# Kernel tuning notes

Hardware: AMD Instinct MI355X
Metric: run time of the kernel (lower is better)

The kernel has to match this reference:

```python
import jax, jax.numpy as jnp
import numpy as np

D_MODEL = 256
N_HEADS = 8
WS = 4          # window size
SHIFTED = True
HEAD_DIM = D_MODEL // N_HEADS


def _shift_masks(ws):
    # Masks for the last row / last column of windows after the cyclic shift
    # (standard from-scratch Swin shifted-window mask construction).
    T = ws * ws
    s = ws * (ws // 2)
    row = np.zeros((T, T), np.float32)
    row[-s:, :-s] = -np.inf
    row[:-s, -s:] = -np.inf
    # einops '(r w1) (c w2) -> (w1 r) (w2 c)' with w1=w2=ws
    col = row.reshape(ws, ws, ws, ws).transpose(1, 0, 3, 2).reshape(T, T)
    return jnp.asarray(row), jnp.asarray(col)


def setup_inputs() -> dict:
    key = jax.random.key(0)
    kx, kw, kb = jax.random.split(key, 3)
    x = jax.random.normal(kx, (32, 56 * 56, D_MODEL), jnp.float32)
    W = jax.random.normal(kw, (D_MODEL, 3 * D_MODEL), jnp.float32) * 0.02
    b = jax.random.normal(kb, (3 * D_MODEL,), jnp.float32) * 0.02
    return {"x": x, "W": W, "b": b}


def reference(x, W, b):
    B, L, D = x.shape
    h = w = int(np.sqrt(L))
    ws, nh, hd = WS, N_HEADS, HEAD_DIM
    # QKV projection; torch code splits last dim as (heads, head_dim, 3) -> K innermost
    qkv = (x @ W + b).reshape(B, h, w, nh, hd, 3)
    if SHIFTED:
        qkv = jnp.roll(qkv, (-(ws // 2), -(ws // 2)), axis=(1, 2))
    nwh, nww = h // ws, w // ws
    # window partition: b (i m1) (j m2) n e k -> b n i j (m1 m2) e k
    qkv = qkv.reshape(B, nwh, ws, nww, ws, nh, hd, 3)
    qkv = qkv.transpose(0, 5, 1, 3, 2, 4, 6, 7).reshape(B, nh, nwh, nww, ws * ws, hd, 3)
    q, k, v = qkv[..., 0], qkv[..., 1], qkv[..., 2]
    scores = jnp.einsum('bnijte,bnijse->bnijts', q, k) / jnp.sqrt(jnp.float32(hd))
    if SHIFTED:
        row_mask, col_mask = _shift_masks(ws)
        scores = scores.at[:, :, -1, :].add(row_mask)   # last row of windows
        scores = scores.at[:, :, :, -1].add(col_mask)   # last column of windows
    att = jax.nn.softmax(scores, axis=-1)
    out = jnp.einsum('bnijts,bnijse->bnijte', att, v)
    # reverse window partition: b n i j (m1 m2) e -> b (i m1) (j m2) (n e)
    out = out.reshape(B, nh, nwh, nww, ws, ws, hd)
    out = out.transpose(0, 2, 4, 3, 5, 1, 6).reshape(B, h, w, D)
    if SHIFTED:
        out = jnp.roll(out, (ws // 2, ws // 2), axis=(1, 2))
    return out.reshape(B, L, D)
```

## Files before the change

kernel.cpp:

```cpp
#include <hip/hip_runtime.h>

typedef __attribute__((ext_vector_type(8))) short short8;
typedef __attribute__((ext_vector_type(4))) short short4v;
typedef __attribute__((ext_vector_type(4))) float floatx4;

#define NWSIDE 14
#define HLEN   56
#define DM     256

#define QK_STRIDE 264
#define K_OFF     4224
#define VT_OFF    8448
#define WINELEMS  12544

static __device__ __forceinline__ unsigned int f2bfu(float f) {
    unsigned int u = __float_as_uint(f);
    return (u + 0x7fffu + ((u >> 16) & 1u)) >> 16;
}
static __device__ __forceinline__ unsigned short f2bf(float f) {
    return (unsigned short)f2bfu(f);
}

__global__ void swin_prep(const float* __restrict__ W, const float* __restrict__ bias,
                          unsigned short* __restrict__ Wt, float* __restrict__ bperm) {
    const int k = blockIdx.x;
    const int ks = k >> 5, lq = (k >> 3) & 3, j = k & 7;
    #pragma unroll
    for (int it = 0; it < 3; ++it) {
        const int c = it * 256 + threadIdx.x;
        const float w = W[(size_t)k * 768 + c];
        const int h = c / 96, r = c - h * 96;
        const int e = r / 3, sect = r - e * 3;
        const int cp = h * 96 + sect * 32 + e;
        const int t = cp >> 4, lrow = cp & 15;
        Wt[(size_t)(((t * 8 + ks) * 64 + lq * 16 + lrow) << 3) + j] = f2bf(w);
        if (k == 0) bperm[cp] = bias[c];
    }
}

__global__ __launch_bounds__(256, 3)
void swin_mfma(const float* __restrict__ x,
               const unsigned short* __restrict__ Wt,
               const float* __restrict__ bperm,
               float* __restrict__ out) {
    __shared__ __align__(16) unsigned short lds[2 * WINELEMS];

    const int b    = blockIdx.x / 98;
    const int g    = blockIdx.x % 98;
    const int tid  = threadIdx.x;
    const int wv   = tid >> 6;
    const int lane = tid & 63;
    const int lrow = lane & 15;
    const int lq   = lane >> 4;
    const float scale = 0.17677669529663687f;
    const floatx4 zf = {0.f, 0.f, 0.f, 0.f};

    const int u2 = tid >> 7, tk = (tid >> 3) & 15, sg = tid & 7;
    const int ww2 = g * 2 + u2;
    const int wi2 = ww2 / NWSIDE, wj2 = ww2 % NWSIDE;
    const int gr2 = (wi2 * 4 + (tk >> 2) + 2) % HLEN;
    const int gc2 = (wj2 * 4 + (tk & 3) + 2) % HLEN;
    const size_t rowoff = ((size_t)(b * 3136 + gr2 * 56 + gc2)) * DM;

    {
        const floatx4* xr = (const floatx4*)(x + rowoff);
        unsigned short* xd = &lds[u2 * WINELEMS + tk * QK_STRIDE];
        #pragma unroll
        for (int j = 0; j < 8; ++j) {
            floatx4 f = xr[sg + 8 * j];
            short4v p;
            p[0] = (short)f2bf(f[0]); p[1] = (short)f2bf(f[1]);
            p[2] = (short)f2bf(f[2]); p[3] = (short)f2bf(f[3]);
            *(short4v*)&xd[(sg + 8 * j) * 4] = p;
        }
    }
    __syncthreads();

    const unsigned short* wfp = Wt + (size_t)(wv * 12) * 4096 + (size_t)lane * 8;
    short8 Ac[8], An[8];
    #pragma unroll
    for (int ks = 0; ks < 8; ++ks) Ac[ks] = *(const short8*)(wfp + ks * 512);
    floatx4 bc = *(const floatx4*)&bperm[wv * 12 * 16 + lq * 4];
    floatx4 bn;

    short8 xf[2][8];
    #pragma unroll
    for (int u = 0; u < 2; ++u)
        #pragma unroll
        for (int ks = 0; ks < 8; ++ks)
            xf[u][ks] = *(const short8*)&lds[u * WINELEMS + lrow * QK_STRIDE + ks * 32 + lq * 8];
    __syncthreads();

    #pragma unroll
    for (int n = 0; n < 12; ++n) {
        const int t    = wv * 12 + n;
        const int col0 = t * 16;

        if (n < 11) {
            const unsigned short* wnp = wfp + (size_t)(n + 1) * 4096;
            #pragma unroll
            for (int ks = 0; ks < 8; ++ks) An[ks] = *(const short8*)(wnp + ks * 512);
            bn = *(const floatx4*)&bperm[(t + 1) * 16 + lq * 4];
        }

        floatx4 acc0 = bc, acc1 = bc;
        #pragma unroll
        for (int ks = 0; ks < 8; ++ks) {
            acc0 = __builtin_amdgcn_mfma_f32_16x16x32_bf16(Ac[ks], xf[0][ks], acc0, 0, 0, 0);
            acc1 = __builtin_amdgcn_mfma_f32_16x16x32_bf16(Ac[ks], xf[1][ks], acc1, 0, 0, 0);
        }

        const int h    = t / 6;
        const int r    = col0 - h * 96;
        const int sect = r >> 5;
        const int e0   = r & 31;
        if (sect < 2) {
            const int base = (sect ? K_OFF : 0) + lrow * QK_STRIDE + h * 32 + e0 + lq * 4;
            short4v p0, p1;
            p0[0] = (short)f2bf(acc0[0]); p0[1] = (short)f2bf(acc0[1]);
            p0[2] = (short)f2bf(acc0[2]); p0[3] = (short)f2bf(acc0[3]);
            p1[0] = (short)f2bf(acc1[0]); p1[1] = (short)f2bf(acc1[1]);
            p1[2] = (short)f2bf(acc1[2]); p1[3] = (short)f2bf(acc1[3]);
            *(short4v*)&lds[base]            = p0;
            *(short4v*)&lds[WINELEMS + base] = p1;
        } else {
            #pragma unroll
            for (int i = 0; i < 4; ++i) {
                const int rowe = h * 32 + e0 + lq * 4 + i;
                lds[VT_OFF + rowe * 16 + lrow]            = f2bf(acc0[i]);
                lds[WINELEMS + VT_OFF + rowe * 16 + lrow] = f2bf(acc1[i]);
            }
        }

        if (n < 11) {
            #pragma unroll
            for (int ks = 0; ks < 8; ++ks) Ac[ks] = An[ks];
            bc = bn;
        }
    }
    __syncthreads();

    const int u     = wv >> 1;
    const int hbase = (wv & 1) * 4;
    const int ww = g * 2 + u;
    const int wi = ww / NWSIDE, wj = ww % NWSIDE;
    const bool lastrow = (wi == NWSIDE - 1);
    const bool lastcol = (wj == NWSIDE - 1);
    const unsigned short* wl = lds + u * WINELEMS;
    const bool mrow = lastrow && ((lrow >= 8) != (lq >= 2));
    const bool mc   = ((lrow & 3) >= 2);
    const int vtq = (lq & 1) * 8;

    floatx4 ST[4];
    #pragma unroll
    for (int hh = 0; hh < 4; ++hh) {
        const int h = hbase + hh;
        short8 Ak = *(const short8*)&wl[K_OFF + lrow * QK_STRIDE + h * 32 + lq * 8];
        short8 Bq = *(const short8*)&wl[lrow * QK_STRIDE + h * 32 + lq * 8];
        ST[hh] = __builtin_amdgcn_mfma_f32_16x16x32_bf16(Ak, Bq, zf, 0, 0, 0);
    }

    const int gr5 = (wi * 4 + (lrow >> 2) + 2) % HLEN;
    const int gc5 = (wj * 4 + (lrow & 3) + 2) % HLEN;
    float* op = out + ((size_t)(b * 3136 + gr5 * 56 + gc5)) * DM;

    #pragma unroll
    for (int hh = 0; hh < 4; ++hh) {
        const int h = hbase + hh;
        float ev[4];
        #pragma unroll
        for (int i = 0; i < 4; ++i) {
            bool m = mrow || (lastcol && (mc != (i >= 2)));
            ev[i] = __expf(m ? -1e30f : ST[hh][i] * scale);
        }
        float rs = (ev[0] + ev[1]) + (ev[2] + ev[3]);
        rs += __shfl_xor(rs, 16);
        rs += __shfl_xor(rs, 32);
        const float inv = 1.0f / rs;
        const unsigned int d0 = f2bfu(ev[0] * inv) | (f2bfu(ev[1] * inv) << 16);
        const unsigned int d1 = f2bfu(ev[2] * inv) | (f2bfu(ev[3] * inv) << 16);
        const int src0 = lrow + ((lq & 1) << 5);
        int b0 = __shfl((int)d0, src0);
        int b1 = __shfl((int)d1, src0);
        int b2 = __shfl((int)d0, src0 + 16);
        int b3 = __shfl((int)d1, src0 + 16);
        if (lq >= 2) { b0 = 0; b1 = 0; b2 = 0; b3 = 0; }
        union { int i4[4]; short8 s8; } bp;
        bp.i4[0] = b0; bp.i4[1] = b1; bp.i4[2] = b2; bp.i4[3] = b3;
        #pragma unroll
        for (int eb = 0; eb < 2; ++eb) {
            short8 Av = *(const short8*)&wl[VT_OFF + (h * 32 + eb * 16 + lrow) * 16 + vtq];
            floatx4 O = __builtin_amdgcn_mfma_f32_16x16x32_bf16(Av, bp.s8, zf, 0, 0, 0);
            *(floatx4*)&op[h * 32 + eb * 16 + lq * 4] = O;
        }
    }
}

extern "C" void kernel_launch(void* const* d_in, const int* in_sizes, int n_in,
                              void* d_out, int out_size, void* d_ws, size_t ws_size,
                              hipStream_t stream) {
    const float* x    = (const float*)d_in[0];
    const float* W    = (const float*)d_in[1];
    const float* bias = (const float*)d_in[2];
    float* out = (float*)d_out;
    (void)in_sizes; (void)n_in; (void)out_size; (void)ws_size;

    unsigned short* Wt = (unsigned short*)d_ws;
    float* bperm = (float*)((char*)d_ws + 768 * 256 * 2);

    swin_prep<<<256, 256, 0, stream>>>(W, bias, Wt, bperm);
    swin_mfma<<<32 * 98, 256, 0, stream>>>(x, Wt, bperm, out);
}
```

Baseline: 223.8 us.

## Split QKV projection into QK then V phases to shrink LDS and registers

The projection is restructured so Q and K tiles are computed first, the QK^T scores are taken, and V^T is then computed into the LDS region that held K. This cuts per-block LDS from two 12544-element windows to two 8448-element windows. The weight prefetch is reduced from a double-buffered 8-fragment set to a 4-deep rotating buffer with bias added after accumulation, which lowers register pressure. Launch bounds rise to 4 blocks per CU. The cost is an extra __syncthreads and a serialized V phase after the scores.

```diff
diff --git a/kernel.cpp b/kernel.cpp
--- a/kernel.cpp
+++ b/kernel.cpp
@@ -10,8 +10,8 @@
 
 #define QK_STRIDE 264
 #define K_OFF     4224
-#define VT_OFF    8448
-#define WINELEMS  12544
+#define VT_OFF    4224
+#define WINB      8448
 
 static __device__ __forceinline__ unsigned int f2bfu(float f) {
     unsigned int u = __float_as_uint(f);
@@ -38,12 +38,12 @@
     }
 }
 
-__global__ __launch_bounds__(256, 3)
+__global__ __launch_bounds__(256, 4)
 void swin_mfma(const float* __restrict__ x,
                const unsigned short* __restrict__ Wt,
                const float* __restrict__ bperm,
                float* __restrict__ out) {
-    __shared__ __align__(16) unsigned short lds[2 * WINELEMS];
+    __shared__ __align__(16) unsigned short lds[2 * WINB];
 
     const int b    = blockIdx.x / 98;
     const int g    = blockIdx.x % 98;
@@ -64,7 +64,7 @@
 
     {
         const floatx4* xr = (const floatx4*)(x + rowoff);
-        unsigned short* xd = &lds[u2 * WINELEMS + tk * QK_STRIDE];
+        unsigned short* xd = &lds[u2 * WINB + tk * QK_STRIDE];
         #pragma unroll
         for (int j = 0; j < 8; ++j) {
             floatx4 f = xr[sg + 8 * j];
@@ -76,68 +76,55 @@
     }
     __syncthreads();
 
-    const unsigned short* wfp = Wt + (size_t)(wv * 12) * 4096 + (size_t)lane * 8;
-    short8 Ac[8], An[8];
-    #pragma unroll
-    for (int ks = 0; ks < 8; ++ks) Ac[ks] = *(const short8*)(wfp + ks * 512);
-    floatx4 bc = *(const floatx4*)&bperm[wv * 12 * 16 + lq * 4];
-    floatx4 bn;
+    const unsigned short* wbase = Wt + (size_t)(96 * wv) * 512 + (size_t)(lane * 8);
+
+    short8 Ab[4];
+    #pragma unroll
+    for (int f = 0; f < 4; ++f)
+        Ab[f] = *(const short8*)(wbase + (f << 9));
 
     short8 xf[2][8];
     #pragma unroll
     for (int u = 0; u < 2; ++u)
         #pragma unroll
         for (int ks = 0; ks < 8; ++ks)
-            xf[u][ks] = *(const short8*)&lds[u * WINELEMS + lrow * QK_STRIDE + ks * 32 + lq * 8];
-    __syncthreads();
-
-    #pragma unroll
-    for (int n = 0; n < 12; ++n) {
-        const int t    = wv * 12 + n;
-        const int col0 = t * 16;
-
-        if (n < 11) {
-            const unsigned short* wnp = wfp + (size_t)(n + 1) * 4096;
-            #pragma unroll
-            for (int ks = 0; ks < 8; ++ks) An[ks] = *(const short8*)(wnp + ks * 512);
-            bn = *(const floatx4*)&bperm[(t + 1) * 16 + lq * 4];
-        }
-
-        floatx4 acc0 = bc, acc1 = bc;
-        #pragma unroll
-        for (int ks = 0; ks < 8; ++ks) {
-            acc0 = __builtin_amdgcn_mfma_f32_16x16x32_bf16(Ac[ks], xf[0][ks], acc0, 0, 0, 0);
-            acc1 = __builtin_amdgcn_mfma_f32_16x16x32_bf16(Ac[ks], xf[1][ks], acc1, 0, 0, 0);
-        }
-
-        const int h    = t / 6;
-        const int r    = col0 - h * 96;
-        const int sect = r >> 5;
-        const int e0   = r & 31;
-        if (sect < 2) {
+            xf[u][ks] = *(const short8*)&lds[u * WINB + lrow * QK_STRIDE + ks * 32 + lq * 8];
+    __syncthreads();
+
+    floatx4 acc0, acc1, bcv;
+    #pragma unroll
+    for (int f = 0; f < 64; ++f) {
+        const int pi = f >> 3, ks = f & 7;
+        if (ks == 0) {
+            const int t = 12 * wv + 6 * (pi >> 2) + (pi & 3);
+            bcv = *(const floatx4*)&bperm[t * 16 + lq * 4];
+            acc0 = zf; acc1 = zf;
+        }
+        const short8 a = Ab[f & 3];
+        if (f + 4 < 64) {
+            const int pn = (f + 4) >> 3, kn = (f + 4) & 7;
+            Ab[f & 3] = *(const short8*)(wbase + ((48 * (pn >> 2) + 8 * (pn & 3) + kn) << 9));
+        }
+        acc0 = __builtin_amdgcn_mfma_f32_16x16x32_bf16(a, xf[0][ks], acc0, 0, 0, 0);
+        acc1 = __builtin_amdgcn_mfma_f32_16x16x32_bf16(a, xf[1][ks], acc1, 0, 0, 0);
+        if (ks == 7) {
+            const int h    = 2 * wv + (pi >> 2);
+            const int sect = (pi >> 1) & 1;
+            const int e0   = (pi & 1) * 16;
             const int base = (sect ? K_OFF : 0) + lrow * QK_STRIDE + h * 32 + e0 + lq * 4;
             short4v p0, p1;
-            p0[0] = (short)f2bf(acc0[0]); p0[1] = (short)f2bf(acc0[1]);
-            p0[2] = (short)f2bf(acc0[2]); p0[3] = (short)f2bf(acc0[3]);
-            p1[0] = (short)f2bf(acc1[0]); p1[1] = (short)f2bf(acc1[1]);
-            p1[2] = (short)f2bf(acc1[2]); p1[3] = (short)f2bf(acc1[3]);
-            *(short4v*)&lds[base]            = p0;
-            *(short4v*)&lds[WINELEMS + base] = p1;
-        } else {
-            #pragma unroll
-            for (int i = 0; i < 4; ++i) {
-                const int rowe = h * 32 + e0 + lq * 4 + i;
-                lds[VT_OFF + rowe * 16 + lrow]            = f2bf(acc0[i]);
-                lds[WINELEMS + VT_OFF + rowe * 16 + lrow] = f2bf(acc1[i]);
-            }
-        }
-
-        if (n < 11) {
-            #pragma unroll
-            for (int ks = 0; ks < 8; ++ks) Ac[ks] = An[ks];
-            bc = bn;
-        }
-    }
+            p0[0] = (short)f2bf(acc0[0] + bcv[0]); p0[1] = (short)f2bf(acc0[1] + bcv[1]);
+            p0[2] = (short)f2bf(acc0[2] + bcv[2]); p0[3] = (short)f2bf(acc0[3] + bcv[3]);
+            p1[0] = (short)f2bf(acc1[0] + bcv[0]); p1[1] = (short)f2bf(acc1[1] + bcv[1]);
+            p1[2] = (short)f2bf(acc1[2] + bcv[2]); p1[3] = (short)f2bf(acc1[3] + bcv[3]);
+            *(short4v*)&lds[base]        = p0;
+            *(short4v*)&lds[WINB + base] = p1;
+        }
+    }
+
+    #pragma unroll
+    for (int f = 0; f < 4; ++f)
+        Ab[f] = *(const short8*)(wbase + ((32 + f) << 9));
     __syncthreads();
 
     const int u     = wv >> 1;
@@ -146,7 +133,7 @@
     const int wi = ww / NWSIDE, wj = ww % NWSIDE;
     const bool lastrow = (wi == NWSIDE - 1);
     const bool lastcol = (wj == NWSIDE - 1);
-    const unsigned short* wl = lds + u * WINELEMS;
+    const unsigned short* wl = lds + u * WINB;
     const bool mrow = lastrow && ((lrow >= 8) != (lq >= 2));
     const bool mc   = ((lrow & 3) >= 2);
     const int vtq = (lq & 1) * 8;
@@ -159,6 +146,35 @@
         short8 Bq = *(const short8*)&wl[lrow * QK_STRIDE + h * 32 + lq * 8];
         ST[hh] = __builtin_amdgcn_mfma_f32_16x16x32_bf16(Ak, Bq, zf, 0, 0, 0);
     }
+    __syncthreads();
+
+    #pragma unroll
+    for (int f = 0; f < 32; ++f) {
+        const int pi = f >> 3, ks = f & 7;
+        if (ks == 0) {
+            const int t = 12 * wv + 6 * (pi >> 1) + 4 + (pi & 1);
+            bcv = *(const floatx4*)&bperm[t * 16 + lq * 4];
+            acc0 = zf; acc1 = zf;
+        }
+        const short8 a = Ab[f & 3];
+        if (f + 4 < 32) {
+            const int pn = (f + 4) >> 3, kn = (f + 4) & 7;
+            Ab[f & 3] = *(const short8*)(wbase + ((48 * (pn >> 1) + 32 + 8 * (pn & 1) + kn) << 9));
+        }
+        acc0 = __builtin_amdgcn_mfma_f32_16x16x32_bf16(a, xf[0][ks], acc0, 0, 0, 0);
+        acc1 = __builtin_amdgcn_mfma_f32_16x16x32_bf16(a, xf[1][ks], acc1, 0, 0, 0);
+        if (ks == 7) {
+            const int h  = 2 * wv + (pi >> 1);
+            const int e0 = (pi & 1) * 16;
+            #pragma unroll
+            for (int i = 0; i < 4; ++i) {
+                const int rowe = h * 32 + e0 + lq * 4 + i;
+                lds[VT_OFF + rowe * 16 + lrow]        = f2bf(acc0[i] + bcv[i]);
+                lds[WINB + VT_OFF + rowe * 16 + lrow] = f2bf(acc1[i] + bcv[i]);
+            }
+        }
+    }
+    __syncthreads();
 
     const int gr5 = (wi * 4 + (lrow >> 2) + 2) % HLEN;
     const int gc5 = (wj * 4 + (lrow & 3) + 2) % HLEN;
```

Result: slower. 256.9 us (+14.8%).
